# Kernel tuning notes

Measured on AMD Instinct MI355X. Metric: run time of the kernel, lower is better.

Reference implementation:

```python
import jax, jax.numpy as jnp
import numpy as np

B, T, D, K, DEPTH = 8, 1024, 128, 64, 1


def _rel_ids(T, k):
    # relative_mat_id[i, j] = clamp(k + j - i, 0, 2k)
    base = jnp.arange(k, k + T)[None, :] - jnp.arange(T)[:, None]
    return jnp.clip(base, 0, 2 * k)  # [T, T] int32


def setup_inputs() -> dict:
    key = jax.random.key(0)
    ks = jax.random.split(key, 13)
    s = 1.0 / np.sqrt(D)
    return {
        "x": jax.random.normal(ks[0], (B, T, D), dtype=jnp.float32),
        "W0": jax.random.normal(ks[1], (D, D), dtype=jnp.float32) * s,
        "b0": jnp.zeros((D,), dtype=jnp.float32),
        "Wq": jax.random.normal(ks[2], (D, D), dtype=jnp.float32) * s,
        "bq": jnp.zeros((D,), dtype=jnp.float32),
        "Wk": jax.random.normal(ks[3], (D, D), dtype=jnp.float32) * s,
        "bk": jnp.zeros((D,), dtype=jnp.float32),
        "Wv": jax.random.normal(ks[4], (D, D), dtype=jnp.float32) * s,
        "bv": jnp.zeros((D,), dtype=jnp.float32),
        "W1": jax.random.normal(ks[5], (D, D), dtype=jnp.float32) * s,
        "b1": jnp.zeros((D,), dtype=jnp.float32),
        "pe_key": jax.random.normal(ks[6], (2 * K + 1, D), dtype=jnp.float32) * np.sqrt(2.0 / (2 * K + 1)),
        "pe_value": jax.random.normal(ks[7], (2 * K + 1, D), dtype=jnp.float32) * np.sqrt(2.0 / (2 * K + 1)),
    }


def reference(x, W0, b0, Wq, bq, Wk, bk, Wv, bv, W1, b1, pe_key, pe_value):
    Tlen = x.shape[1]
    ids = _rel_ids(Tlen, K)                     # [T, T]
    rpr_key = pe_key[ids]                       # [T, T, D]
    rpr_value = pe_value[ids]                   # [T, T, D]

    hs = jax.nn.relu(x @ W0 + b0)               # fc0 (dropout = eval identity)
    for _ in range(DEPTH):
        q = jnp.tanh(hs @ Wq + bq)
        k = jnp.tanh(hs @ Wk + bk)
        v = jnp.tanh(hs @ Wv + bv)
        a = jnp.einsum("bid,bjd->bij", q, k)
        a = a + jnp.einsum("ijd,bid->bij", rpr_key, q)
        a = jax.nn.softmax(a, axis=2)
        c = jnp.einsum("bij,bjd->bid", a, v)
        c = c + jnp.einsum("bij,ijd->bid", a, rpr_value)
        hs = jax.nn.relu(c @ W1 + b1)
    return hs
```

## Files before the change

kernel.cpp:

```cpp
#include <hip/hip_runtime.h>


#define TT 1024
#define DD 128
#define NB 8
#define SJH 1160

typedef _Float16 f16;
typedef __attribute__((ext_vector_type(8))) _Float16 f16x8;
typedef __attribute__((ext_vector_type(4))) _Float16 f16x4;
typedef __attribute__((ext_vector_type(4))) float f32x4;

static __device__ inline float fast_tanh(float x) {
    float xc = fminf(fmaxf(x, -12.f), 12.f);
    float e = __expf(2.f * xc);
    return (e - 1.f) / (e + 1.f);
}

#define GLDS(gp, lp) __builtin_amdgcn_global_load_lds( \
    (const __attribute__((address_space(1))) unsigned*)(gp), \
    (__attribute__((address_space(3))) unsigned*)(lp), 16, 0, 0)

__global__ __launch_bounds__(256) void prep_all(
        const float* __restrict__ W0, const float* __restrict__ Wq,
        const float* __restrict__ Wk, const float* __restrict__ Wv,
        const float* __restrict__ W1, const float* __restrict__ PEK,
        const float* __restrict__ PEV, char* __restrict__ wimg,
        char* __restrict__ pekimg, char* __restrict__ pevimg) {
    const int blk = blockIdx.x, t = threadIdx.x;
    if (blk < 5) {
        const float* W = blk == 0 ? W0 : blk == 1 ? Wq : blk == 2 ? Wk
                       : blk == 3 ? Wv : W1;
        char* o = wimg + (size_t)blk * 32768;
        #pragma unroll
        for (int it = 0; it < 8; it++) {
            int item = t + 256 * it;
            int n = item & 127, k0 = (item >> 7) * 8;
            f16x8 h;
            #pragma unroll
            for (int e = 0; e < 8; e++) h[e] = (f16)W[(k0 + e) * 128 + n];
            *(f16x8*)(o + n * 256 + ((2 * k0) ^ ((n & 7) << 4))) = h;
        }
    } else if (blk == 5) {
        for (int it = 0; it < 64; it++) {
            int idx = t + 256 * it;
            int m = idx >> 7, d = idx & 127;
            *(f16*)(pekimg + (m >> 6) * 16384 + (m & 63) * 256
                    + ((2 * d) ^ ((m & 7) << 4))) = (f16)PEK[m * 128 + d];
        }
    } else {
        for (int it = 0; it < 64; it++) {
            int idx = t + 256 * it;
            int m = idx >> 7, d = idx & 127;
            *(f16*)(pevimg + (m >> 6) * 16384 + d * 128
                    + ((2 * (m & 63)) ^ ((d & 7) << 4))) = (f16)PEV[m * 128 + d];
        }
    }
}

#define ZACC() do { _Pragma("unroll") for (int _i = 0; _i < 2; _i++) \
    _Pragma("unroll") for (int _j = 0; _j < 2; _j++) \
        acc[_i][_j] = (f32x4){0.f, 0.f, 0.f, 0.f}; } while (0)

#define GEMMCORE(SRC, WL) do { \
    _Pragma("unroll") for (int _c = 0; _c < 4; _c++) { \
        f16x8 _af[2], _bf[2]; \
        _Pragma("unroll") for (int _it = 0; _it < 2; _it++) { \
            int _row = _it * 16 + (l & 15); \
            int _a = (_row << 8) + (_c << 6) + ((l >> 4) << 4); \
            _af[_it] = *(const f16x8*)((SRC) + (_a ^ ((_row & 7) << 4))); } \
        _Pragma("unroll") for (int _nt = 0; _nt < 2; _nt++) { \
            int _n = wv * 32 + _nt * 16 + (l & 15); \
            int _a = (_n << 8) + (_c << 6) + ((l >> 4) << 4); \
            _bf[_nt] = *(const f16x8*)((WL) + (_a ^ ((_n & 7) << 4))); } \
        _Pragma("unroll") for (int _it = 0; _it < 2; _it++) \
        _Pragma("unroll") for (int _nt = 0; _nt < 2; _nt++) \
            acc[_it][_nt] = __builtin_amdgcn_mfma_f32_16x16x32_f16( \
                    _af[_it], _bf[_nt], acc[_it][_nt], 0, 0, 0); } } while (0)

#define ISSUEW(wi, dst) do { \
    const char* _g = wimg + (size_t)(wi) * 32768 + t * 16; \
    char* _d = (dst) + t * 16; \
    _Pragma("unroll") for (int _i = 0; _i < 8; _i++) \
        GLDS(_g + _i * 4096, _d + _i * 4096); \
} while (0)

#define WAITBAR(N) do { \
    asm volatile("s_waitcnt vmcnt(" #N ") lgkmcnt(0)" ::: "memory"); \
    __builtin_amdgcn_s_barrier(); \
    __builtin_amdgcn_sched_barrier(0); \
} while (0)

__global__ __launch_bounds__(256) void fused_qkv(
        const float* __restrict__ x, const char* __restrict__ wimg,
        const float* __restrict__ b0, const float* __restrict__ bq,
        const float* __restrict__ bk, const float* __restrict__ bv,
        f16* __restrict__ q16, char* __restrict__ kimg,
        char* __restrict__ vimg) {
    extern __shared__ __align__(16) char smq[];
    char* xs  = smq;
    char* hsl = smq + 8192;
    char* wA  = smq + 16384;
    char* wB  = smq + 49152;
    char* wC  = smq + 81920;
    const int t = threadIdx.x, wv = t >> 6, l = t & 63;
    const int blk = blockIdx.x;

    const int r0 = (blk & 7) * 1024 + (blk >> 3) * 32;
    ISSUEW(0, wA);
    ISSUEW(1, wB);
    {
        const float* X = x + (size_t)r0 * 128;
        #pragma unroll
        for (int i = 0; i < 2; i++) {
            f32x4 a0 = *(const f32x4*)(X + t * 16 + i * 8);
            f32x4 a1 = *(const f32x4*)(X + t * 16 + i * 8 + 4);
            f16x8 h;
            h[0]=(f16)a0[0]; h[1]=(f16)a0[1]; h[2]=(f16)a0[2]; h[3]=(f16)a0[3];
            h[4]=(f16)a1[0]; h[5]=(f16)a1[1]; h[6]=(f16)a1[2]; h[7]=(f16)a1[3];
            int a = t * 32 + i * 16;
            *(f16x8*)(xs + (a ^ (((a >> 8) & 7) << 4))) = h;
        }
    }
    WAITBAR(8);

    f32x4 acc[2][2];
    ZACC();
    GEMMCORE(xs, wA);
    {
        #pragma unroll
        for (int it = 0; it < 2; it++)
            #pragma unroll
            for (int nt = 0; nt < 2; nt++) {
                int n = wv * 32 + nt * 16 + (l & 15);
                float bb = b0[n];
                #pragma unroll
                for (int r = 0; r < 4; r++) {
                    int i = it * 16 + (l >> 4) * 4 + r;
                    float v = fmaxf(acc[it][nt][r] + bb, 0.f);
                    int a = i * 256 + 2 * n;
                    *(f16*)(hsl + (a ^ ((i & 7) << 4))) = (f16)v;
                }
            }
    }
    ISSUEW(2, wC);
    WAITBAR(8);

    ZACC();
    GEMMCORE(hsl, wB);
    {
        #pragma unroll
        for (int it = 0; it < 2; it++)
            #pragma unroll
            for (int nt = 0; nt < 2; nt++) {
                int n = wv * 32 + nt * 16 + (l & 15);
                float bb = bq[n];
                #pragma unroll
                for (int r = 0; r < 4; r++) {
                    int i = it * 16 + (l >> 4) * 4 + r;
                    q16[(size_t)(r0 + i) * 128 + n] =
                            (f16)fast_tanh(acc[it][nt][r] + bb);
                }
            }
    }
    ISSUEW(3, wA);
    WAITBAR(8);

    ZACC();
    GEMMCORE(hsl, wC);
    f16* ts = (f16*)xs;
    {
        #pragma unroll
        for (int it = 0; it < 2; it++)
            #pragma unroll
            for (int nt = 0; nt < 2; nt++) {
                int n = wv * 32 + nt * 16 + (l & 15);
                float bb = bk[n];
                #pragma unroll
                for (int r = 0; r < 4; r++) {
                    int i = it * 16 + (l >> 4) * 4 + r;
                    ts[i * 128 + n] = (f16)fast_tanh(acc[it][nt][r] + bb);
                }
            }
    }
    WAITBAR(0);

    {
        #pragma unroll
        for (int half = 0; half < 2; half++) {
            int row = (t >> 4) + half * 16;
            int seg = t & 15;
            int jg = r0 + row;
            int chunk = ((jg >> 10) << 4) + ((jg & 1023) >> 6);
            int jp = jg & 63;
            char* dst = kimg + (size_t)chunk * 16384 + jp * 256
                      + ((seg * 16) ^ ((jp & 7) << 4));
            *(f16x8*)dst = *(const f16x8*)&ts[row * 128 + seg * 8];
        }
    }
    ZACC();
    GEMMCORE(hsl, wA);
    {
        #pragma unroll
        for (int it = 0; it < 2; it++)
            #pragma unroll
            for (int nt = 0; nt < 2; nt++) {
                int d = wv * 32 + nt * 16 + (l & 15);
                float bb = bv[d];
                f16x4 h;
                #pragma unroll
                for (int r = 0; r < 4; r++)
                    h[r] = (f16)fast_tanh(acc[it][nt][r] + bb);
                int jb = r0 + it * 16 + ((l >> 4) << 2);
                int chunk = ((jb >> 10) << 4) + ((jb & 1023) >> 6);
                char* dst = vimg + (size_t)chunk * 16384 + d * 128
                          + ((2 * (jb & 63)) ^ ((d & 7) << 4));
                *(f16x4*)dst = h;
            }
    }
}

#define ISSUE16(src, bi) do { const char* _g = (src) + t * 16; \
    char* _d = BUF + (size_t)(bi) * 16384 + t * 16; \
    GLDS(_g, _d); GLDS(_g + 4096, _d + 4096); \
    GLDS(_g + 8192, _d + 8192); GLDS(_g + 12288, _d + 12288); \
} while (0)

__global__ __launch_bounds__(256) void attn_all(
        const f16* __restrict__ q16, const char* __restrict__ kimg,
        const char* __restrict__ pekimg, const char* __restrict__ vimg,
        const char* __restrict__ pevimg, const float* __restrict__ PEK,
        const float* __restrict__ PEV, const char* __restrict__ w1img,
        const float* __restrict__ b1, float* __restrict__ out) {
    extern __shared__ __align__(16) char sm7[];
    f16*   S   = (f16*)sm7;
    char*  BUF = sm7 + 37120;
    f16*   QB  = (f16*)(sm7 + 69888);
    float* LR  = (float*)(sm7 + 74112);

    const int t = threadIdx.x, wv = t >> 6, l = t & 63;
    const int lr = l & 15, lg = l >> 4;
    const int b = blockIdx.x & 7;
    const int i0 = (blockIdx.x >> 3) << 4;

    f16x8 qf[4];
    {
        const f16* qb = q16 + (size_t)(b * TT + i0 + lr) * 128 + lg * 8;
        #pragma unroll
        for (int c = 0; c < 4; c++) qf[c] = *(const f16x8*)(qb + c * 32);
    }
    const int row2 = t >> 4, l16 = t & 15;
    f16x8 qpv = *(const f16x8*)(q16 + (size_t)(b * TT + i0 + row2) * 128 + l16 * 8);
    f32x4 pkv0 = *(const f32x4*)(PEK + 128 * 128 + l16 * 8);
    f32x4 pkv1 = *(const f32x4*)(PEK + 128 * 128 + l16 * 8 + 4);
    f32x4 pvr4[2];
    #pragma unroll
    for (int dt = 0; dt < 2; dt++)
        pvr4[dt] = *(const f32x4*)(PEV + 128 * 128 + wv * 32 + dt * 16 + lg * 4);
    float bb1[2];
    #pragma unroll
    for (int nt = 0; nt < 2; nt++) bb1[nt] = b1[wv * 32 + nt * 16 + lr];

    const char* kbase = kimg + (size_t)b * 16 * 16384;
    const char* vbase = vimg + (size_t)b * 16 * 16384;

    ISSUE16(kbase, 0);

    for (int ch = 0; ch < 18; ch++) {
        asm volatile("s_waitcnt vmcnt(0)" ::: "memory");
        __builtin_amdgcn_s_barrier();
        __builtin_amdgcn_sched_barrier(0);
        {
            int ci = ch + 1;
            const char* src = ci < 16 ? kbase + (size_t)ci * 16384
                            : (ci < 18 ? pekimg + (size_t)(ci - 16) * 16384
                                       : vbase);
            ISSUE16(src, ci & 1);
        }
        const char* kb = BUF + (size_t)(ch & 1) * 16384;
        const int jp = wv * 16 + lr;
        f32x4 a2 = {0.f, 0.f, 0.f, 0.f};
        #pragma unroll
        for (int c = 0; c < 4; c++) {
            f16x8 kf = *(const f16x8*)(kb + jp * 256
                        + ((c * 64 + lg * 16) ^ ((jp & 7) << 4)));
            a2 = __builtin_amdgcn_mfma_f32_16x16x32_f16(kf, qf[c], a2, 0, 0, 0);
        }
        f16x4 h = {(f16)a2[0], (f16)a2[1], (f16)a2[2], (f16)a2[3]};
        *(f16x4*)&S[lr * SJH + ch * 64 + wv * 16 + lg * 4] = h;
    }
    asm volatile("s_waitcnt lgkmcnt(0)" ::: "memory");
    __builtin_amdgcn_s_barrier();
    __builtin_amdgcn_sched_barrier(0);

    {
        const int ig = i0 + row2;
        f16* srow = S + row2 * SJH;
        f16* qrow = QB + row2 * 132;

        float qp;
        {
            float s = 0.f;
            #pragma unroll
            for (int e = 0; e < 4; e++) s += (float)qpv[e] * pkv0[e];
            #pragma unroll
            for (int e = 0; e < 4; e++) s += (float)qpv[e + 4] * pkv1[e];
            #pragma unroll
            for (int off = 8; off; off >>= 1) s += __shfl_xor(s, off, 64);
            qp = s;
        }
        for (int mm = l16; mm < 128; mm += 16) {
            qrow[mm] = srow[1024 + mm];
            srow[1024 + mm] = (f16)0.f;
        }
        if (l16 == 0) qrow[128] = (f16)qp;
        const float qlo = (float)qrow[0], qhi = qp;

        float lmax = -3.0e38f;
        #pragma unroll
        for (int kk = 0; kk < 8; kk++) {
            int j0 = kk * 128 + l16 * 8;
            f16x8 sv = *(const f16x8*)(srow + j0);
            #pragma unroll
            for (int e = 0; e < 8; e++) {
                int idd = 64 + j0 + e - ig;
                float qv = (idd <= 0) ? qlo : (idd >= 128 ? qhi : (float)qrow[idd]);
                lmax = fmaxf(lmax, (float)sv[e] + qv);
            }
        }
        #pragma unroll
        for (int off = 8; off; off >>= 1) lmax = fmaxf(lmax, __shfl_xor(lmax, off, 64));

        float lsum = 0.f, s0 = 0.f, s1 = 0.f;
        #pragma unroll
        for (int kk = 0; kk < 8; kk++) {
            int j0 = kk * 128 + l16 * 8;
            f16x8 sv = *(const f16x8*)(srow + j0);
            f16x8 pv;
            #pragma unroll
            for (int e = 0; e < 8; e++) {
                int idd = 64 + j0 + e - ig;
                float qv = (idd <= 0) ? qlo : (idd >= 128 ? qhi : (float)qrow[idd]);
                float p = __expf((float)sv[e] + qv - lmax);
                pv[e] = (f16)p;
                lsum += p;
                if (idd <= 0)        s0 += p;
                else if (idd >= 128) s1 += p;
                else                 srow[1024 + idd] = (f16)p;
            }
            *(f16x8*)(srow + j0) = pv;
        }
        #pragma unroll
        for (int off = 8; off; off >>= 1) {
            lsum += __shfl_xor(lsum, off, 64);
            s0   += __shfl_xor(s0,   off, 64);
            s1   += __shfl_xor(s1,   off, 64);
        }
        if (l16 == 0) {
            srow[1024] = (f16)s0;
            srow[1152] = (f16)s1;
            LR[row2] = lsum;
        }
    }
    asm volatile("s_waitcnt lgkmcnt(0)" ::: "memory");
    __builtin_amdgcn_s_barrier();
    __builtin_amdgcn_sched_barrier(0);

    f32x4 cacc[2] = {};
    for (int ch = 0; ch < 18; ch++) {
        asm volatile("s_waitcnt vmcnt(0)" ::: "memory");
        __builtin_amdgcn_s_barrier();
        __builtin_amdgcn_sched_barrier(0);
        {
            int ci = ch + 1;
            if (ci < 16)      ISSUE16(vbase + (size_t)ci * 16384, ci & 1);
            else if (ci < 18) ISSUE16(pevimg + (size_t)(ci - 16) * 16384, ci & 1);
            else {
                const char* _g = w1img + t * 16;
                char* _d = BUF + t * 16;
                GLDS(_g, _d); GLDS(_g + 4096, _d + 4096);
                GLDS(_g + 8192, _d + 8192); GLDS(_g + 12288, _d + 12288);
            }
        }
        const char* vb = BUF + (size_t)(ch & 1) * 16384;
        #pragma unroll
        for (int c2 = 0; c2 < 2; c2++) {
            f16x8 pf = *(const f16x8*)&S[lr * SJH + ch * 64 + c2 * 32 + lg * 8];
            #pragma unroll
            for (int dt = 0; dt < 2; dt++) {
                int dp = wv * 32 + dt * 16 + lr;
                f16x8 vf = *(const f16x8*)(vb + dp * 128
                            + ((c2 * 64 + lg * 16) ^ ((dp & 7) << 4)));
                cacc[dt] = __builtin_amdgcn_mfma_f32_16x16x32_f16(vf, pf, cacc[dt], 0, 0, 0);
            }
        }
    }

    const float w128 = (float)S[lr * SJH + 1152];
    const float rden = 1.f / LR[lr];
    asm volatile("s_waitcnt lgkmcnt(0)" ::: "memory");
    __builtin_amdgcn_s_barrier();
    __builtin_amdgcn_sched_barrier(0);
    {
        const char* _g = w1img + 16384 + t * 16;
        char* _d = BUF + 16384 + t * 16;
        GLDS(_g, _d); GLDS(_g + 4096, _d + 4096);
        GLDS(_g + 8192, _d + 8192); GLDS(_g + 12288, _d + 12288);
    }
    char* cl = (char*)S;
    #pragma unroll
    for (int dt = 0; dt < 2; dt++) {
        #pragma unroll
        for (int r = 0; r < 4; r++) {
            int d = wv * 32 + dt * 16 + lg * 4 + r;
            float cv = (cacc[dt][r] + w128 * pvr4[dt][r]) * rden;
            int a = lr * 256 + 2 * d;
            *(f16*)(cl + (a ^ ((lr & 7) << 4))) = (f16)cv;
        }
    }
    asm volatile("s_waitcnt vmcnt(0) lgkmcnt(0)" ::: "memory");
    __builtin_amdgcn_s_barrier();
    __builtin_amdgcn_sched_barrier(0);

    const char* wl4 = BUF;
    f32x4 oacc[2] = {};
    #pragma unroll
    for (int c = 0; c < 4; c++) {
        int aa = lr * 256 + c * 64 + lg * 16;
        f16x8 af = *(const f16x8*)(cl + (aa ^ ((lr & 7) << 4)));
        #pragma unroll
        for (int nt = 0; nt < 2; nt++) {
            int n = wv * 32 + nt * 16 + lr;
            int ba = n * 256 + c * 64 + lg * 16;
            f16x8 bf = *(const f16x8*)(wl4 + (ba ^ ((n & 7) << 4)));
            oacc[nt] = __builtin_amdgcn_mfma_f32_16x16x32_f16(af, bf, oacc[nt], 0, 0, 0);
        }
    }
    #pragma unroll
    for (int nt = 0; nt < 2; nt++) {
        int n = wv * 32 + nt * 16 + lr;
        #pragma unroll
        for (int r = 0; r < 4; r++) {
            int i = lg * 4 + r;
            out[(size_t)(b * TT + i0 + i) * DD + n] = fmaxf(oacc[nt][r] + bb1[nt], 0.f);
        }
    }
}


extern "C" void kernel_launch(void* const* d_in, const int* in_sizes, int n_in,
                              void* d_out, int out_size, void* d_ws, size_t ws_size,
                              hipStream_t stream) {
    const float* x   = (const float*)d_in[0];
    const float* W0  = (const float*)d_in[1];
    const float* b0  = (const float*)d_in[2];
    const float* Wq  = (const float*)d_in[3];
    const float* bq  = (const float*)d_in[4];
    const float* Wk  = (const float*)d_in[5];
    const float* bk  = (const float*)d_in[6];
    const float* Wv  = (const float*)d_in[7];
    const float* bv  = (const float*)d_in[8];
    const float* W1  = (const float*)d_in[9];
    const float* b1  = (const float*)d_in[10];
    const float* pek = (const float*)d_in[11];
    const float* pev = (const float*)d_in[12];
    float* out = (float*)d_out;

    const size_t NTD = (size_t)NB * TT * DD;
    f16* q16     = (f16*)d_ws;
    char* wimg   = (char*)(q16 + NTD);
    char* kimg   = wimg + 5 * 32768;
    char* vimg   = kimg + (size_t)128 * 16384;
    char* pekimg = vimg + (size_t)128 * 16384;
    char* pevimg = pekimg + 32768;

    const int SMEM_QKV  = 114688;
    const int SMEM_ATTN = 74176;
    hipFuncSetAttribute(reinterpret_cast<const void*>(fused_qkv),
                        hipFuncAttributeMaxDynamicSharedMemorySize, SMEM_QKV);
    hipFuncSetAttribute(reinterpret_cast<const void*>(attn_all),
                        hipFuncAttributeMaxDynamicSharedMemorySize, SMEM_ATTN);

    hipLaunchKernelGGL(prep_all, dim3(7), dim3(256), 0, stream,
                       W0, Wq, Wk, Wv, W1, pek, pev, wimg, pekimg, pevimg);
    hipLaunchKernelGGL(fused_qkv, dim3(256), dim3(256), SMEM_QKV, stream,
                       x, wimg, b0, bq, bk, bv, q16, kimg, vimg);
    hipLaunchKernelGGL(attn_all, dim3(512), dim3(256), SMEM_ATTN, stream,
                       q16, kimg, pekimg, vimg, pevimg, pek, pev,
                       wimg + 4 * 32768, b1, out);
}
```

Measured before the change: 50.76 us.

## Split V/PEV streaming into 8KB chunks with a four-slot three-deep prefetch ring

Changes the V and PEV images to 32-row 8KB chunks with matching swizzle. The PV loop now streams 36 half-size chunks through a four-slot ring with three chunks in flight and waits on vmcnt(4) rather than draining all loads each step. The aim is to overlap global-to-LDS loads with MFMA work instead of a full wait per chunk. The cost is twice as many barriers per loop and finer MFMA granularity per step.

```diff
diff --git a/kernel.cpp b/kernel.cpp
--- a/kernel.cpp
+++ b/kernel.cpp
@@ -52,8 +52,8 @@
         for (int it = 0; it < 64; it++) {
             int idx = t + 256 * it;
             int m = idx >> 7, d = idx & 127;
-            *(f16*)(pevimg + (m >> 6) * 16384 + d * 128
-                    + ((2 * (m & 63)) ^ ((d & 7) << 4))) = (f16)PEV[m * 128 + d];
+            *(f16*)(pevimg + (m >> 5) * 8192 + d * 64
+                    + ((2 * (m & 31)) ^ ((d & 3) << 4))) = (f16)PEV[m * 128 + d];
         }
     }
 }
@@ -212,9 +212,9 @@
                 for (int r = 0; r < 4; r++)
                     h[r] = (f16)fast_tanh(acc[it][nt][r] + bb);
                 int jb = r0 + it * 16 + ((l >> 4) << 2);
-                int chunk = ((jb >> 10) << 4) + ((jb & 1023) >> 6);
-                char* dst = vimg + (size_t)chunk * 16384 + d * 128
-                          + ((2 * (jb & 63)) ^ ((d & 7) << 4));
+                int chunk = ((jb >> 10) << 5) + ((jb & 1023) >> 5);
+                char* dst = vimg + (size_t)chunk * 8192 + d * 64
+                          + ((2 * (jb & 31)) ^ ((d & 3) << 4));
                 *(f16x4*)dst = h;
             }
     }
@@ -224,6 +224,11 @@
     char* _d = BUF + (size_t)(bi) * 16384 + t * 16; \
     GLDS(_g, _d); GLDS(_g + 4096, _d + 4096); \
     GLDS(_g + 8192, _d + 8192); GLDS(_g + 12288, _d + 12288); \
+} while (0)
+
+#define ISSUE8(src, s8) do { const char* _g = (src) + t * 16; \
+    char* _d = BUF + (size_t)(s8) * 8192 + t * 16; \
+    GLDS(_g, _d); GLDS(_g + 4096, _d + 4096); \
 } while (0)
 
 __global__ __launch_bounds__(256) void attn_all(
@@ -262,7 +267,7 @@
     for (int nt = 0; nt < 2; nt++) bb1[nt] = b1[wv * 32 + nt * 16 + lr];
 
     const char* kbase = kimg + (size_t)b * 16 * 16384;
-    const char* vbase = vimg + (size_t)b * 16 * 16384;
+    const char* vbase = vimg + (size_t)b * 32 * 8192;
 
     ISSUE16(kbase, 0);
 
@@ -272,10 +277,12 @@
         __builtin_amdgcn_sched_barrier(0);
         {
             int ci = ch + 1;
-            const char* src = ci < 16 ? kbase + (size_t)ci * 16384
-                            : (ci < 18 ? pekimg + (size_t)(ci - 16) * 16384
-                                       : vbase);
-            ISSUE16(src, ci & 1);
+            if (ci < 16)      ISSUE16(kbase + (size_t)ci * 16384, ci & 1);
+            else if (ci < 18) ISSUE16(pekimg + (size_t)(ci - 16) * 16384, ci & 1);
+            else {
+                ISSUE8(vbase, 0);
+                ISSUE8(vbase + 8192, 1);
+            }
         }
         const char* kb = BUF + (size_t)(ch & 1) * 16384;
         const int jp = wv * 16 + lr;
@@ -365,34 +372,27 @@
     asm volatile("s_waitcnt lgkmcnt(0)" ::: "memory");
     __builtin_amdgcn_s_barrier();
     __builtin_amdgcn_sched_barrier(0);
+    ISSUE8(vbase + 2 * 8192, 2);
 
     f32x4 cacc[2] = {};
-    for (int ch = 0; ch < 18; ch++) {
-        asm volatile("s_waitcnt vmcnt(0)" ::: "memory");
+    for (int ch = 0; ch < 36; ch++) {
+        asm volatile("s_waitcnt vmcnt(4)" ::: "memory");
         __builtin_amdgcn_s_barrier();
         __builtin_amdgcn_sched_barrier(0);
         {
-            int ci = ch + 1;
-            if (ci < 16)      ISSUE16(vbase + (size_t)ci * 16384, ci & 1);
-            else if (ci < 18) ISSUE16(pevimg + (size_t)(ci - 16) * 16384, ci & 1);
-            else {
-                const char* _g = w1img + t * 16;
-                char* _d = BUF + t * 16;
-                GLDS(_g, _d); GLDS(_g + 4096, _d + 4096);
-                GLDS(_g + 8192, _d + 8192); GLDS(_g + 12288, _d + 12288);
-            }
-        }
-        const char* vb = BUF + (size_t)(ch & 1) * 16384;
-        #pragma unroll
-        for (int c2 = 0; c2 < 2; c2++) {
-            f16x8 pf = *(const f16x8*)&S[lr * SJH + ch * 64 + c2 * 32 + lg * 8];
-            #pragma unroll
-            for (int dt = 0; dt < 2; dt++) {
-                int dp = wv * 32 + dt * 16 + lr;
-                f16x8 vf = *(const f16x8*)(vb + dp * 128
-                            + ((c2 * 64 + lg * 16) ^ ((dp & 7) << 4)));
-                cacc[dt] = __builtin_amdgcn_mfma_f32_16x16x32_f16(vf, pf, cacc[dt], 0, 0, 0);
-            }
+            int ci = ch + 3;
+            if (ci < 32)      ISSUE8(vbase + (size_t)ci * 8192, ci & 3);
+            else if (ci < 36) ISSUE8(pevimg + (size_t)(ci - 32) * 8192, ci & 3);
+            else              ISSUE8(w1img + (size_t)(ci - 36) * 8192, ci & 3);
+        }
+        const char* vb = BUF + (size_t)(ch & 3) * 8192;
+        f16x8 pf = *(const f16x8*)&S[lr * SJH + ch * 32 + lg * 8];
+        #pragma unroll
+        for (int dt = 0; dt < 2; dt++) {
+            int dp = wv * 32 + dt * 16 + lr;
+            f16x8 vf = *(const f16x8*)(vb + dp * 64
+                        + ((lg * 16) ^ ((dp & 3) << 4)));
+            cacc[dt] = __builtin_amdgcn_mfma_f32_16x16x32_f16(vf, pf, cacc[dt], 0, 0, 0);
         }
     }
 
@@ -401,12 +401,7 @@
     asm volatile("s_waitcnt lgkmcnt(0)" ::: "memory");
     __builtin_amdgcn_s_barrier();
     __builtin_amdgcn_sched_barrier(0);
-    {
-        const char* _g = w1img + 16384 + t * 16;
-        char* _d = BUF + 16384 + t * 16;
-        GLDS(_g, _d); GLDS(_g + 4096, _d + 4096);
-        GLDS(_g + 8192, _d + 8192); GLDS(_g + 12288, _d + 12288);
-    }
+    ISSUE8(w1img + 3 * 8192, 3);
     char* cl = (char*)S;
     #pragma unroll
     for (int dt = 0; dt < 2; dt++) {
@@ -471,7 +466,7 @@
     char* wimg   = (char*)(q16 + NTD);
     char* kimg   = wimg + 5 * 32768;
     char* vimg   = kimg + (size_t)128 * 16384;
-    char* pekimg = vimg + (size_t)128 * 16384;
+    char* pekimg = vimg + (size_t)256 * 8192;
     char* pevimg = pekimg + 32768;
 
     const int SMEM_QKV  = 114688;
```

Result: no change. 51.06 us (+0.6%).
